# Kernel optimization log

Hardware: AMD Instinct MI355X
Metric: run time of the kernel (lower is better)

Reference implementation:

```python
import jax, jax.numpy as jnp
import numpy as np

B = 32768   # batch of states (original forward is per-state; we vmap)
D = 3       # coord_dim

_W_SHAPES = [("w_h0",(3,32)),("w_y0",(3,32)),("w_yu0",(3,3)),("w_u0",(3,32)),
             ("w_h1",(32,32)),("w_z1",(32,32)),("w_zu1",(32,32)),("w_y1",(3,32)),
             ("w_yu1",(32,3)),("w_u1",(32,32)),("w_h2",(32,32)),("w_z2",(32,32)),
             ("w_zu2",(32,32)),("w_y2",(3,32)),("w_yu2",(32,3)),("w_u2",(32,32)),
             ("w_z_out",(32,1)),("w_zu_out",(32,32)),("w_y_out",(3,1)),
             ("w_yu_out",(32,3)),("w_u_out",(32,1))]
_B_SHAPES = [("b_y0",(3,)),("b_h0",(32,)),("b_0",(32,)),("b_h1",(32,)),("b_y1",(3,)),
             ("b_z1",(32,)),("b_1",(32,)),("b_h2",(32,)),("b_z2",(32,)),("b_y2",(3,)),
             ("b_2",(32,)),("b_z_out",(32,)),("b_y_out",(3,)),("b_out",(1,))]

def _make_params(key):
    n = len(_W_SHAPES) + len(_B_SHAPES) + 4
    ks = jax.random.split(key, n)
    p, i = {}, 0
    for name, sh in _W_SHAPES:   # torch .uniform_(-0.1, 0.1)
        p[name] = jax.random.uniform(ks[i], sh, jnp.float32, -0.1, 0.1); i += 1
    for name, sh in _B_SHAPES:   # torch.rand -> U[0,1)
        p[name] = jax.random.uniform(ks[i], sh, jnp.float32, 0.0, 1.0); i += 1
    # fc layers: normal init per _init_weights (stds / sqrt(16)=4), zero bias
    stds = [2.2/4.0, 0.58/4.0, 0.58*2.0/4.0, 4.0]
    shapes = [(32, 3), (32, 32), (32, 32), (1, 32)]
    for j in range(4):
        p[f"fc{j+1}_w"] = stds[j] * jax.random.normal(ks[i], shapes[j], jnp.float32); i += 1
        p[f"fc{j+1}_b"] = jnp.zeros((shapes[j][0],), jnp.float32)
    return p

def setup_inputs():
    key = jax.random.key(0)
    kx, kp = jax.random.split(key)
    inp = {"x": jax.random.normal(kx, (B, 2 * D), jnp.float32)}
    inp.update(_make_params(kp))
    return inp

def _forward(x, p):
    sp, relu = jax.nn.softplus, jax.nn.relu

    def lagr(state):
        q, y = state[:D], state[D:]
        u1 = sp(q @ p["w_h0"] + p["b_h0"])
        z1 = sp((y * (q @ p["w_yu0"] + p["b_y0"])) @ p["w_y0"] + q @ p["w_u0"] + p["b_0"])
        u2 = sp(u1 @ p["w_h1"] + p["b_h1"])
        z2 = sp((z1 * (u1 @ p["w_zu1"] + p["b_z1"])) @ relu(p["w_z1"])
                + (y * (u1 @ p["w_yu1"] + p["b_y1"])) @ p["w_y1"]
                + u1 @ p["w_u1"] + p["b_1"])
        u3 = sp(u2 @ p["w_h2"] + p["b_h2"])
        z3 = sp((z2 * (u2 @ p["w_zu2"] + p["b_z2"])) @ relu(p["w_z2"])
                + (y * (u2 @ p["w_yu2"] + p["b_y2"])) @ p["w_y2"]
                + u2 @ p["w_u2"] + p["b_2"])
        zout = sp((z3 * (u3 @ p["w_zu_out"] + p["b_z_out"])) @ relu(p["w_z_out"])
                  + (y * (u3 @ p["w_yu_out"] + p["b_y_out"])) @ p["w_y_out"]
                  + u3 @ p["w_u_out"] + p["b_out"])
        V = sp(q @ p["fc1_w"].T + p["fc1_b"])
        V = sp(V @ p["fc2_w"].T + p["fc2_b"])
        V = sp(V @ p["fc3_w"].T + p["fc3_b"])
        V = V @ p["fc4_w"].T + p["fc4_b"]
        return (zout - V)[0]  # scalar Lagrangian

    def step(state):
        dq = state[D:]
        H = jax.hessian(lagr)(state)        # (6,6)
        g = jax.grad(lagr)(state)[:D]       # dL/dq, matches jacobian row b[0,:3]
        M = H[D:, D:]                       # d2L/ddq ddq
        C = H[D:, :D]                       # d2L/ddq dq
        ddq = (g - dq @ C.T) @ jnp.linalg.inv(M).T
        dx = jnp.concatenate([dq, ddq])
        return state + 0.001 * dx           # Euler step, as in torch forward

    return jax.vmap(step)(x)

def reference(x, w_h0, w_y0, w_yu0, w_u0, w_h1, w_z1, w_zu1, w_y1, w_yu1, w_u1,
              w_h2, w_z2, w_zu2, w_y2, w_yu2, w_u2, w_z_out, w_zu_out, w_y_out,
              w_yu_out, w_u_out, b_y0, b_h0, b_0, b_h1, b_y1, b_z1, b_1, b_h2,
              b_z2, b_y2, b_2, b_z_out, b_y_out, b_out, fc1_w, fc1_b, fc2_w,
              fc2_b, fc3_w, fc3_b, fc4_w, fc4_b):
    p = dict(locals())
    xv = p.pop("x")
    return _forward(xv, p)
```

## Files before the change

### kernel.cpp

```cpp
#include <hip/hip_runtime.h>

#define NTH 64
#define B_TOTAL 32768
#define PSTR 20

typedef float v2f __attribute__((ext_vector_type(2)));
typedef float v4f __attribute__((ext_vector_type(4)));
typedef double v4d __attribute__((ext_vector_type(4)));

struct Ptrs { const float* p[44]; };

enum : int {
  I_X = 0,
  I_WH0 = 1, I_WY0 = 2, I_WYU0 = 3, I_WU0 = 4,
  I_WH1 = 5, I_WZ1 = 6, I_WZU1 = 7, I_WY1 = 8, I_WYU1 = 9, I_WU1 = 10,
  I_WH2 = 11, I_WZ2 = 12, I_WZU2 = 13, I_WY2 = 14, I_WYU2 = 15, I_WU2 = 16,
  I_WZO = 17, I_WZUO = 18, I_WYO = 19, I_WYUO = 20, I_WUO = 21,
  I_BY0 = 22, I_BH0 = 23, I_B0 = 24, I_BH1 = 25, I_BY1 = 26, I_BZ1 = 27, I_B1 = 28,
  I_BH2 = 29, I_BZ2 = 30, I_BY2 = 31, I_B2 = 32, I_BZO = 33, I_BYO = 34, I_BOUT = 35,
  I_FC1 = 36, I_FC1B = 37, I_FC2 = 38, I_FC2B = 39, I_FC3 = 40, I_FC3B = 41,
  I_FC4 = 42, I_FC4B = 43
};

struct V16 { float c[16]; };

__device__ __forceinline__ float spf(float x) {
  return fmaxf(x, 0.0f) + __logf(1.0f + __expf(-fabsf(x)));
}
__device__ __forceinline__ float sigf(float x) {
  return __fdividef(1.0f, 1.0f + __expf(-x));
}

__device__ __forceinline__ V16 spchain16(const V16& A, float y0, float y1, float y2) {
  V16 Z;
  float s = sigf(A.c[0]);
  float d = s * (1.0f - s);
  Z.c[0] = spf(A.c[0]);
#pragma unroll
  for (int a = 0; a < 3; ++a) Z.c[1 + a] = s * A.c[1 + a];
#pragma unroll
  for (int b = 0; b < 3; ++b) Z.c[4 + b] = s * A.c[4 + b];
  Z.c[7]  = s * A.c[7]  + d * A.c[1] * A.c[1];
  Z.c[8]  = s * A.c[8]  + d * A.c[1] * A.c[2];
  Z.c[9]  = s * A.c[9]  + d * A.c[1] * A.c[3];
  Z.c[10] = s * A.c[10] + d * A.c[2] * A.c[2];
  Z.c[11] = s * A.c[11] + d * A.c[2] * A.c[3];
  Z.c[12] = s * A.c[12] + d * A.c[3] * A.c[3];
  float ydq = y0 * A.c[4] + y1 * A.c[5] + y2 * A.c[6];
#pragma unroll
  for (int a = 0; a < 3; ++a) Z.c[13 + a] = s * A.c[13 + a] + d * A.c[1 + a] * ydq;
  return Z;
}

__device__ __forceinline__ void stageProd(float* row, const V16& Z, float S0, float S1,
                                          float S2, float S3, float y0, float y1, float y2) {
  float z0 = Z.c[0];
  float ysd = y0 * S1 + y1 * S2 + y2 * S3;
  v4f w0 = {z0 * S0, S0 * Z.c[1], S0 * Z.c[2], S0 * Z.c[3]};
  v4f w1 = {z0 * S1 + S0 * Z.c[4], z0 * S2 + S0 * Z.c[5], z0 * S3 + S0 * Z.c[6], S0 * Z.c[7]};
  v4f w2 = {S0 * Z.c[8], S0 * Z.c[9], S0 * Z.c[10], S0 * Z.c[11]};
  v4f w3 = {S0 * Z.c[12], S0 * Z.c[13] + Z.c[1] * ysd, S0 * Z.c[14] + Z.c[2] * ysd,
            S0 * Z.c[15] + Z.c[3] * ysd};
  *(v4f*)(row + 0) = w0;  *(v4f*)(row + 4) = w1;
  *(v4f*)(row + 8) = w2;  *(v4f*)(row + 12) = w3;
}

__device__ __forceinline__ V16 prodZS16(const V16& Z, float S0, float S1, float S2, float S3,
                                        float y0, float y1, float y2) {
  V16 P;
  const float Sq[3] = {S1, S2, S3};
  float ysd = y0 * S1 + y1 * S2 + y2 * S3;
  P.c[0] = Z.c[0] * S0;
#pragma unroll
  for (int a = 0; a < 3; ++a) P.c[1 + a] = S0 * Z.c[1 + a];
#pragma unroll
  for (int b = 0; b < 3; ++b) P.c[4 + b] = Z.c[0] * Sq[b] + S0 * Z.c[4 + b];
#pragma unroll
  for (int t = 0; t < 6; ++t) P.c[7 + t] = S0 * Z.c[7 + t];
#pragma unroll
  for (int a = 0; a < 3; ++a) P.c[13 + a] = S0 * Z.c[13 + a] + Z.c[1 + a] * ysd;
  return P;
}

__device__ __forceinline__ void stageU_all(const float* __restrict__ Wh,
                                           const float* __restrict__ Wzu,
                                           const float* __restrict__ Wu,
                                           const float* __restrict__ Wyu, int j,
                                           const float* us,
                                           v2f& h0, v2f& h1, v2f& s0, v2f& s1,
                                           v2f& w0, v2f& w1,
                                           v2f& ta0, v2f& ta1, v2f& tb0, v2f& tb1,
                                           v2f& tc0, v2f& tc1) {
#pragma unroll 2
  for (int i = 0; i < 32; ++i) {
    v4f u = *(const v4f*)(us + i * 4);
    float wh = Wh[i * 32 + j], wz = Wzu[i * 32 + j], wu = Wu[i * 32 + j];
    h0 += u.xy * wh; h1 += u.zw * wh;
    s0 += u.xy * wz; s1 += u.zw * wz;
    w0 += u.xy * wu; w1 += u.zw * wu;
    float wy0 = Wyu[i * 3 + 0], wy1 = Wyu[i * 3 + 1], wy2 = Wyu[i * 3 + 2];
    ta0 += u.xy * wy0; ta1 += u.zw * wy0;
    tb0 += u.xy * wy1; tb1 += u.zw * wy1;
    tc0 += u.xy * wy2; tc1 += u.zw * wy2;
  }
}

__device__ __forceinline__ void buildA16(const float* __restrict__ Wy, int j, float y0, float y1,
                                         float y2, const float wv[4], const float ta[4],
                                         const float tb[4], const float tc[4], V16& A) {
  float wy0 = Wy[j], wy1 = Wy[32 + j], wy2 = Wy[64 + j];
  A.c[0] = wv[0] + y0 * ta[0] * wy0 + y1 * tb[0] * wy1 + y2 * tc[0] * wy2;
  A.c[1] = ta[0] * wy0; A.c[2] = tb[0] * wy1; A.c[3] = tc[0] * wy2;
#pragma unroll
  for (int b = 0; b < 3; ++b)
    A.c[4 + b] = wv[1 + b] + y0 * ta[1 + b] * wy0 + y1 * tb[1 + b] * wy1 + y2 * tc[1 + b] * wy2;
#pragma unroll
  for (int t6 = 0; t6 < 6; ++t6) A.c[7 + t6] = 0.0f;
  float yta = y0 * ta[1] + y1 * ta[2] + y2 * ta[3];
  float ytb = y0 * tb[1] + y1 * tb[2] + y2 * tb[3];
  float ytc = y0 * tc[1] + y1 * tc[2] + y2 * tc[3];
  A.c[13] = yta * wy0; A.c[14] = ytb * wy1; A.c[15] = ytc * wy2;
}

__global__ __launch_bounds__(NTH, 4) void lnn_step_kernel(Ptrs P, float* __restrict__ out) {
  __shared__ float pstage[2][32][PSTR];
  __shared__ float ustage[2][32][4];

  const int tid = threadIdx.x;
  const int j = tid & 31;
  const int half = tid >> 5;
  const int sample = blockIdx.x * 2 + half;

  float* prow = &pstage[half][0][0];
  float* urow = &ustage[half][0][0];
  float* pst0 = &pstage[0][0][0];
  float* pst1 = &pstage[1][0][0];
  const int l64 = tid & 63;
  const int n16 = l64 & 15;
  const int kq = l64 >> 4;

  const float* X = P.p[I_X] + sample * 6;
  const float q0 = X[0], q1 = X[1], q2 = X[2];
  const float y0 = X[3], y1 = X[4], y2 = X[5];

  float Vg0, Vg1, Vg2;
  {
    const float* fc1 = P.p[I_FC1];
    float f0 = fc1[j * 3], f1 = fc1[j * 3 + 1], f2 = fc1[j * 3 + 2];
    float hp = P.p[I_FC1B][j] + q0 * f0 + q1 * f1 + q2 * f2;
    float ss = sigf(hp);
    *(v4f*)(urow + j * 4) = (v4f){spf(hp), ss * f0, ss * f1, ss * f2};
    const float* fc2 = P.p[I_FC2] + j * 32;
    v2f a0 = {P.p[I_FC2B][j], 0.0f}, a1 = {0.0f, 0.0f};
#pragma unroll 2
    for (int r = 0; r < 8; ++r) {
      v4f w4 = *(const v4f*)(fc2 + r * 4);
      v4f u0 = *(const v4f*)(urow + (r * 4 + 0) * 4);
      v4f u1 = *(const v4f*)(urow + (r * 4 + 1) * 4);
      v4f u2 = *(const v4f*)(urow + (r * 4 + 2) * 4);
      v4f u3 = *(const v4f*)(urow + (r * 4 + 3) * 4);
      a0 += u0.xy * w4.x; a1 += u0.zw * w4.x;
      a0 += u1.xy * w4.y; a1 += u1.zw * w4.y;
      a0 += u2.xy * w4.z; a1 += u2.zw * w4.z;
      a0 += u3.xy * w4.w; a1 += u3.zw * w4.w;
    }
    float ss2 = sigf(a0.x);
    *(v4f*)(urow + j * 4) = (v4f){spf(a0.x), ss2 * a0.y, ss2 * a1.x, ss2 * a1.y};
    const float* fc3 = P.p[I_FC3] + j * 32;
    v2f b0 = {P.p[I_FC3B][j], 0.0f}, b1 = {0.0f, 0.0f};
#pragma unroll 2
    for (int r = 0; r < 8; ++r) {
      v4f w4 = *(const v4f*)(fc3 + r * 4);
      v4f u0 = *(const v4f*)(urow + (r * 4 + 0) * 4);
      v4f u1 = *(const v4f*)(urow + (r * 4 + 1) * 4);
      v4f u2 = *(const v4f*)(urow + (r * 4 + 2) * 4);
      v4f u3 = *(const v4f*)(urow + (r * 4 + 3) * 4);
      b0 += u0.xy * w4.x; b1 += u0.zw * w4.x;
      b0 += u1.xy * w4.y; b1 += u1.zw * w4.y;
      b0 += u2.xy * w4.z; b1 += u2.zw * w4.z;
      b0 += u3.xy * w4.w; b1 += u3.zw * w4.w;
    }
    float ss3 = sigf(b0.x);
    float f4 = P.p[I_FC4][j];
    Vg0 = ss3 * b0.y * f4; Vg1 = ss3 * b1.x * f4; Vg2 = ss3 * b1.y * f4;
  }

  const float* yu0 = P.p[I_WYU0];
  float t0v[3];
#pragma unroll
  for (int k = 0; k < 3; ++k)
    t0v[k] = q0 * yu0[k] + q1 * yu0[3 + k] + q2 * yu0[6 + k] + P.p[I_BY0][k];

  float u1c[4];
  {
    const float* wh0 = P.p[I_WH0];
    float w0 = wh0[j], w1 = wh0[32 + j], w2 = wh0[64 + j];
    float h = P.p[I_BH0][j] + q0 * w0 + q1 * w1 + q2 * w2;
    float ss = sigf(h);
    u1c[0] = spf(h); u1c[1] = ss * w0; u1c[2] = ss * w1; u1c[3] = ss * w2;
  }

  V16 z;
  {
    const float* Wy = P.p[I_WY0];
    const float* Wu = P.p[I_WU0];
    float wy0 = Wy[j], wy1 = Wy[32 + j], wy2 = Wy[64 + j];
    float wu0 = Wu[j], wu1 = Wu[32 + j], wu2 = Wu[64 + j];
    V16 A;
    A.c[0] = P.p[I_B0][j] + (y0 * t0v[0]) * wy0 + (y1 * t0v[1]) * wy1 + (y2 * t0v[2]) * wy2 +
             q0 * wu0 + q1 * wu1 + q2 * wu2;
    A.c[1] = t0v[0] * wy0; A.c[2] = t0v[1] * wy1; A.c[3] = t0v[2] * wy2;
#pragma unroll
    for (int b = 0; b < 3; ++b) {
      float acc = (b == 0 ? wu0 : (b == 1 ? wu1 : wu2));
      acc += y0 * yu0[b * 3 + 0] * wy0 + y1 * yu0[b * 3 + 1] * wy1 + y2 * yu0[b * 3 + 2] * wy2;
      A.c[4 + b] = acc;
    }
#pragma unroll
    for (int t = 0; t < 6; ++t) A.c[7 + t] = 0.0f;
    float yty0 = y0 * yu0[0] + y1 * yu0[3] + y2 * yu0[6];
    float yty1 = y0 * yu0[1] + y1 * yu0[4] + y2 * yu0[7];
    float yty2 = y0 * yu0[2] + y1 * yu0[5] + y2 * yu0[8];
    A.c[13] = yty0 * wy0; A.c[14] = yty1 * wy1; A.c[15] = yty2 * wy2;
    z = spchain16(A, y0, y1, y2);
  }

  float unext[4];
#pragma unroll 1
  for (int lvl = 0; lvl < 2; ++lvl) {
    const float* Wh  = P.p[lvl == 0 ? I_WH1 : I_WH2];
    const float* Wzu = P.p[lvl == 0 ? I_WZU1 : I_WZU2];
    const float* Wu  = P.p[lvl == 0 ? I_WU1 : I_WU2];
    const float* Wyu = P.p[lvl == 0 ? I_WYU1 : I_WYU2];
    const float* Wy  = P.p[lvl == 0 ? I_WY1 : I_WY2];
    const float* Wz  = P.p[lvl == 0 ? I_WZ1 : I_WZ2];
    const float* Bh  = P.p[lvl == 0 ? I_BH1 : I_BH2];
    const float* Bz  = P.p[lvl == 0 ? I_BZ1 : I_BZ2];
    const float* Bl  = P.p[lvl == 0 ? I_B1 : I_B2];
    const float* By  = P.p[lvl == 0 ? I_BY1 : I_BY2];

    const float* uc = (lvl == 0) ? u1c : unext;
    *(v4f*)(urow + j * 4) = (v4f){uc[0], uc[1], uc[2], uc[3]};

    v2f h0 = {Bh[j], 0.0f}, h1 = {0.0f, 0.0f};
    v2f s0 = {Bz[j], 0.0f}, s1 = {0.0f, 0.0f};
    v2f w0 = {Bl[j], 0.0f}, w1 = {0.0f, 0.0f};
    v2f ta0 = {By[0], 0.0f}, ta1 = {0.0f, 0.0f};
    v2f tb0 = {By[1], 0.0f}, tb1 = {0.0f, 0.0f};
    v2f tc0 = {By[2], 0.0f}, tc1 = {0.0f, 0.0f};
    stageU_all(Wh, Wzu, Wu, Wyu, j, urow, h0, h1, s0, s1, w0, w1,
               ta0, ta1, tb0, tb1, tc0, tc1);
    {
      float ss = sigf(h0.x);
      unext[0] = spf(h0.x); unext[1] = ss * h0.y; unext[2] = ss * h1.x; unext[3] = ss * h1.y;
    }
    stageProd(prow + j * PSTR, z, s0.x, s0.y, s1.x, s1.y, y0, y1, y2);

    v4d a00 = {0.0, 0.0, 0.0, 0.0};
    v4d a01 = {0.0, 0.0, 0.0, 0.0};
    v4d a10 = {0.0, 0.0, 0.0, 0.0};
    v4d a11 = {0.0, 0.0, 0.0, 0.0};
#pragma unroll
    for (int c = 0; c < 8; ++c) {
      const int i = c * 4 + kq;
      double b0 = (double)pst0[i * PSTR + n16];
      double b1 = (double)pst1[i * PSTR + n16];
      double wlo = (double)fmaxf(Wz[i * 32 + n16], 0.0f);
      double whi = (double)fmaxf(Wz[i * 32 + 16 + n16], 0.0f);
      a00 = __builtin_amdgcn_mfma_f64_16x16x4f64(wlo, b0, a00, 0, 0, 0);
      a01 = __builtin_amdgcn_mfma_f64_16x16x4f64(whi, b0, a01, 0, 0, 0);
      a10 = __builtin_amdgcn_mfma_f64_16x16x4f64(wlo, b1, a10, 0, 0, 0);
      a11 = __builtin_amdgcn_mfma_f64_16x16x4f64(whi, b1, a11, 0, 0, 0);
    }
#pragma unroll
    for (int r = 0; r < 4; ++r) {
      pst0[(kq + 4 * r) * PSTR + n16]        = (float)a00[r];
      pst0[(16 + kq + 4 * r) * PSTR + n16]   = (float)a01[r];
      pst1[(kq + 4 * r) * PSTR + n16]        = (float)a10[r];
      pst1[(16 + kq + 4 * r) * PSTR + n16]   = (float)a11[r];
    }

    float wvv[4] = {w0.x, w0.y, w1.x, w1.y};
    float tav[4] = {ta0.x, ta0.y, ta1.x, ta1.y};
    float tbv[4] = {tb0.x, tb0.y, tb1.x, tb1.y};
    float tcv[4] = {tc0.x, tc0.y, tc1.x, tc1.y};
    V16 A2;
    buildA16(Wy, j, y0, y1, y2, wvv, tav, tbv, tcv, A2);

    {
      const float* rown = prow + j * PSTR;
      v4f r0 = *(const v4f*)(rown + 0);
      v4f r1 = *(const v4f*)(rown + 4);
      v4f r2 = *(const v4f*)(rown + 8);
      v4f r3 = *(const v4f*)(rown + 12);
      A2.c[0] += r0.x;  A2.c[1] += r0.y;  A2.c[2] += r0.z;  A2.c[3] += r0.w;
      A2.c[4] += r1.x;  A2.c[5] += r1.y;  A2.c[6] += r1.z;  A2.c[7] += r1.w;
      A2.c[8] += r2.x;  A2.c[9] += r2.y;  A2.c[10] += r2.z; A2.c[11] += r2.w;
      A2.c[12] += r3.x; A2.c[13] += r3.y; A2.c[14] += r3.z; A2.c[15] += r3.w;
    }
    z = spchain16(A2, y0, y1, y2);
  }

  *(v4f*)(urow + j * 4) = (v4f){unext[0], unext[1], unext[2], unext[3]};
  v2f s30 = {P.p[I_BZO][j], 0.0f}, s31 = {0.0f, 0.0f};
  v2f wo0 = {0.0f, 0.0f}, wo1 = {0.0f, 0.0f};
  v2f t3a0 = {P.p[I_BYO][0], 0.0f}, t3a1 = {0.0f, 0.0f};
  v2f t3b0 = {P.p[I_BYO][1], 0.0f}, t3b1 = {0.0f, 0.0f};
  v2f t3c0 = {P.p[I_BYO][2], 0.0f}, t3c1 = {0.0f, 0.0f};
  {
    const float* Wzuo = P.p[I_WZUO];
    const float* Wuo = P.p[I_WUO];
    const float* Wyuo = P.p[I_WYUO];
#pragma unroll 2
    for (int i = 0; i < 32; ++i) {
      v4f u = *(const v4f*)(urow + i * 4);
      float wz = Wzuo[i * 32 + j];
      s30 += u.xy * wz; s31 += u.zw * wz;
      float wu = Wuo[i];
      wo0 += u.xy * wu; wo1 += u.zw * wu;
      float wy0 = Wyuo[i * 3], wy1 = Wyuo[i * 3 + 1], wy2 = Wyuo[i * 3 + 2];
      t3a0 += u.xy * wy0; t3a1 += u.zw * wy0;
      t3b0 += u.xy * wy1; t3b1 += u.zw * wy1;
      t3c0 += u.xy * wy2; t3c1 += u.zw * wy2;
    }
  }
  const float woc[4] = {wo0.x, wo0.y, wo1.x, wo1.y};
  const float t3av[4] = {t3a0.x, t3a0.y, t3a1.x, t3a1.y};
  const float t3bv[4] = {t3b0.x, t3b0.y, t3b1.x, t3b1.y};
  const float t3cv[4] = {t3c0.x, t3c0.y, t3c1.x, t3c1.y};

  float red[19];
  {
    V16 p3 = prodZS16(z, s30.x, s30.y, s31.x, s31.y, y0, y1, y2);
    float wz = fmaxf(P.p[I_WZO][j], 0.0f);
#pragma unroll
    for (int k = 0; k < 16; ++k) red[k] = p3.c[k] * wz;
    red[16] = Vg0; red[17] = Vg1; red[18] = Vg2;
  }
#pragma unroll
  for (int m = 16; m >= 1; m >>= 1) {
#pragma unroll
    for (int k = 0; k < 19; ++k) red[k] += __shfl_xor(red[k], m, 32);
  }

  if (j == 0) {
    const float* Wyo = P.p[I_WYO];
    const float wyo0 = Wyo[0], wyo1 = Wyo[1], wyo2 = Wyo[2];
    float Av = red[0] + woc[0] + P.p[I_BOUT][0] + y0 * t3av[0] * wyo0 +
               y1 * t3bv[0] * wyo1 + y2 * t3cv[0] * wyo2;
    float Agy[3];
    Agy[0] = red[1] + t3av[0] * wyo0;
    Agy[1] = red[2] + t3bv[0] * wyo1;
    Agy[2] = red[3] + t3cv[0] * wyo2;
    float Agq[3];
#pragma unroll
    for (int b = 0; b < 3; ++b)
      Agq[b] = red[4 + b] + woc[1 + b] + y0 * t3av[1 + b] * wyo0 +
               y1 * t3bv[1 + b] * wyo1 + y2 * t3cv[1 + b] * wyo2;
    float ycq[3];
    ycq[0] = red[13] + (y0 * t3av[1] + y1 * t3av[2] + y2 * t3av[3]) * wyo0;
    ycq[1] = red[14] + (y0 * t3bv[1] + y1 * t3bv[2] + y2 * t3bv[3]) * wyo1;
    ycq[2] = red[15] + (y0 * t3cv[1] + y1 * t3cv[2] + y2 * t3cv[3]) * wyo2;
    float s = sigf(Av), d = s * (1.0f - s);

    double Mm[3][3];
    const int pa[6] = {0, 0, 0, 1, 1, 2}, pb[6] = {0, 1, 2, 1, 2, 2};
#pragma unroll
    for (int t = 0; t < 6; ++t) {
      double m = (double)s * (double)red[7 + t] +
                 (double)d * (double)Agy[pa[t]] * (double)Agy[pb[t]];
      Mm[pa[t]][pb[t]] = m; Mm[pb[t]][pa[t]] = m;
    }
    double yAgq = (double)y0 * (double)Agq[0] + (double)y1 * (double)Agq[1] +
                  (double)y2 * (double)Agq[2];
    double rr[3];
#pragma unroll
    for (int a = 0; a < 3; ++a) {
      double g = (double)s * (double)Agq[a] - (double)red[16 + a];
      double Cy = (double)s * (double)ycq[a] + (double)d * (double)Agy[a] * yAgq;
      rr[a] = g - Cy;
    }
    double a = Mm[0][0], b_ = Mm[0][1], c_ = Mm[0][2], dd = Mm[1][1], e = Mm[1][2], f = Mm[2][2];
    double A00 = dd * f - e * e, A01 = c_ * e - b_ * f, A02 = b_ * e - c_ * dd;
    double A11 = a * f - c_ * c_, A12 = b_ * c_ - a * e, A22 = a * dd - b_ * b_;
    double det = a * A00 + b_ * A01 + c_ * A02;
    double idet = 1.0 / det;
    double d0 = (A00 * rr[0] + A01 * rr[1] + A02 * rr[2]) * idet;
    double d1 = (A01 * rr[0] + A11 * rr[1] + A12 * rr[2]) * idet;
    double d2 = (A02 * rr[0] + A12 * rr[1] + A22 * rr[2]) * idet;

    float* O = out + (size_t)sample * 6;
    O[0] = q0 + 0.001f * y0;
    O[1] = q1 + 0.001f * y1;
    O[2] = q2 + 0.001f * y2;
    O[3] = y0 + 0.001f * (float)d0;
    O[4] = y1 + 0.001f * (float)d1;
    O[5] = y2 + 0.001f * (float)d2;
  }
}

extern "C" void kernel_launch(void* const* d_in, const int* in_sizes, int n_in,
                              void* d_out, int out_size, void* d_ws, size_t ws_size,
                              hipStream_t stream) {
  (void)in_sizes; (void)n_in; (void)d_ws; (void)ws_size; (void)out_size;
  Ptrs P;
  for (int i = 0; i < 44; ++i) P.p[i] = (const float*)d_in[i];
  float* out = (float*)d_out;
  dim3 grid(B_TOTAL / 2), block(NTH);
  hipLaunchKernelGGL(lnn_step_kernel, grid, block, 0, stream, P, out);
}
```

Measured before the change: 130.6 us.

## Process two samples per half-wave to amortize weight loads and MFMA work

Each 32-lane half now handles two samples instead of one, so a 64-thread block covers four samples and the grid is halved. The Wz matrix loads are reused across two MFMA pairs, and per-sample phases are factored into inline helpers. The launch-bounds occupancy hint of 4 is dropped. Live registers per thread roughly double with two V16 states, which may cut occupancy or cause spills, and the serialized per-sample work gives less parallelism per block.

```diff
diff --git a/kernel.cpp b/kernel.cpp
--- a/kernel.cpp
+++ b/kernel.cpp
@@ -122,110 +122,256 @@
   A.c[13] = yta * wy0; A.c[14] = ytb * wy1; A.c[15] = ytc * wy2;
 }
 
-__global__ __launch_bounds__(NTH, 4) void lnn_step_kernel(Ptrs P, float* __restrict__ out) {
-  __shared__ float pstage[2][32][PSTR];
-  __shared__ float ustage[2][32][4];
+__device__ __forceinline__ void vchainVALU(const Ptrs& P, int j, float q0, float q1, float q2,
+                                           float* urow, float& Vg0, float& Vg1, float& Vg2) {
+  const float* fc1 = P.p[I_FC1];
+  float f0 = fc1[j * 3], f1 = fc1[j * 3 + 1], f2 = fc1[j * 3 + 2];
+  float hp = P.p[I_FC1B][j] + q0 * f0 + q1 * f1 + q2 * f2;
+  float ss = sigf(hp);
+  *(v4f*)(urow + j * 4) = (v4f){spf(hp), ss * f0, ss * f1, ss * f2};
+  const float* fc2 = P.p[I_FC2] + j * 32;
+  v2f a0 = {P.p[I_FC2B][j], 0.0f}, a1 = {0.0f, 0.0f};
+#pragma unroll 2
+  for (int r = 0; r < 8; ++r) {
+    v4f w4 = *(const v4f*)(fc2 + r * 4);
+    v4f u0 = *(const v4f*)(urow + (r * 4 + 0) * 4);
+    v4f u1 = *(const v4f*)(urow + (r * 4 + 1) * 4);
+    v4f u2 = *(const v4f*)(urow + (r * 4 + 2) * 4);
+    v4f u3 = *(const v4f*)(urow + (r * 4 + 3) * 4);
+    a0 += u0.xy * w4.x; a1 += u0.zw * w4.x;
+    a0 += u1.xy * w4.y; a1 += u1.zw * w4.y;
+    a0 += u2.xy * w4.z; a1 += u2.zw * w4.z;
+    a0 += u3.xy * w4.w; a1 += u3.zw * w4.w;
+  }
+  float ss2 = sigf(a0.x);
+  *(v4f*)(urow + j * 4) = (v4f){spf(a0.x), ss2 * a0.y, ss2 * a1.x, ss2 * a1.y};
+  const float* fc3 = P.p[I_FC3] + j * 32;
+  v2f b0 = {P.p[I_FC3B][j], 0.0f}, b1 = {0.0f, 0.0f};
+#pragma unroll 2
+  for (int r = 0; r < 8; ++r) {
+    v4f w4 = *(const v4f*)(fc3 + r * 4);
+    v4f u0 = *(const v4f*)(urow + (r * 4 + 0) * 4);
+    v4f u1 = *(const v4f*)(urow + (r * 4 + 1) * 4);
+    v4f u2 = *(const v4f*)(urow + (r * 4 + 2) * 4);
+    v4f u3 = *(const v4f*)(urow + (r * 4 + 3) * 4);
+    b0 += u0.xy * w4.x; b1 += u0.zw * w4.x;
+    b0 += u1.xy * w4.y; b1 += u1.zw * w4.y;
+    b0 += u2.xy * w4.z; b1 += u2.zw * w4.z;
+    b0 += u3.xy * w4.w; b1 += u3.zw * w4.w;
+  }
+  float ss3 = sigf(b0.x);
+  float f4 = P.p[I_FC4][j];
+  Vg0 = ss3 * b0.y * f4; Vg1 = ss3 * b1.x * f4; Vg2 = ss3 * b1.y * f4;
+}
+
+__device__ __forceinline__ V16 zinit(const Ptrs& P, int j, float q0, float q1, float q2,
+                                     float y0, float y1, float y2) {
+  const float* yu0 = P.p[I_WYU0];
+  float t0v[3];
+#pragma unroll
+  for (int k = 0; k < 3; ++k)
+    t0v[k] = q0 * yu0[k] + q1 * yu0[3 + k] + q2 * yu0[6 + k] + P.p[I_BY0][k];
+  const float* Wy = P.p[I_WY0];
+  const float* Wu = P.p[I_WU0];
+  float wy0 = Wy[j], wy1 = Wy[32 + j], wy2 = Wy[64 + j];
+  float wu0 = Wu[j], wu1 = Wu[32 + j], wu2 = Wu[64 + j];
+  V16 A;
+  A.c[0] = P.p[I_B0][j] + (y0 * t0v[0]) * wy0 + (y1 * t0v[1]) * wy1 + (y2 * t0v[2]) * wy2 +
+           q0 * wu0 + q1 * wu1 + q2 * wu2;
+  A.c[1] = t0v[0] * wy0; A.c[2] = t0v[1] * wy1; A.c[3] = t0v[2] * wy2;
+#pragma unroll
+  for (int b = 0; b < 3; ++b) {
+    float acc = (b == 0 ? wu0 : (b == 1 ? wu1 : wu2));
+    acc += y0 * yu0[b * 3 + 0] * wy0 + y1 * yu0[b * 3 + 1] * wy1 + y2 * yu0[b * 3 + 2] * wy2;
+    A.c[4 + b] = acc;
+  }
+#pragma unroll
+  for (int t = 0; t < 6; ++t) A.c[7 + t] = 0.0f;
+  float yty0 = y0 * yu0[0] + y1 * yu0[3] + y2 * yu0[6];
+  float yty1 = y0 * yu0[1] + y1 * yu0[4] + y2 * yu0[7];
+  float yty2 = y0 * yu0[2] + y1 * yu0[5] + y2 * yu0[8];
+  A.c[13] = yty0 * wy0; A.c[14] = yty1 * wy1; A.c[15] = yty2 * wy2;
+  return spchain16(A, y0, y1, y2);
+}
+
+__device__ __forceinline__ void u1init(const Ptrs& P, int j, float q0, float q1, float q2,
+                                       float u1c[4]) {
+  const float* wh0 = P.p[I_WH0];
+  float w0 = wh0[j], w1 = wh0[32 + j], w2 = wh0[64 + j];
+  float h = P.p[I_BH0][j] + q0 * w0 + q1 * w1 + q2 * w2;
+  float ss = sigf(h);
+  u1c[0] = spf(h); u1c[1] = ss * w0; u1c[2] = ss * w1; u1c[3] = ss * w2;
+}
+
+__device__ __forceinline__ void mv16pair(const float* __restrict__ Wz, int n16, int kq,
+                                         float* pstX, float* pstY) {
+  v4d a00 = {0.0, 0.0, 0.0, 0.0};
+  v4d a01 = {0.0, 0.0, 0.0, 0.0};
+  v4d a10 = {0.0, 0.0, 0.0, 0.0};
+  v4d a11 = {0.0, 0.0, 0.0, 0.0};
+#pragma unroll
+  for (int c = 0; c < 8; ++c) {
+    const int i = c * 4 + kq;
+    double b0 = (double)pstX[i * PSTR + n16];
+    double b1 = (double)pstY[i * PSTR + n16];
+    double wlo = (double)fmaxf(Wz[i * 32 + n16], 0.0f);
+    double whi = (double)fmaxf(Wz[i * 32 + 16 + n16], 0.0f);
+    a00 = __builtin_amdgcn_mfma_f64_16x16x4f64(wlo, b0, a00, 0, 0, 0);
+    a01 = __builtin_amdgcn_mfma_f64_16x16x4f64(whi, b0, a01, 0, 0, 0);
+    a10 = __builtin_amdgcn_mfma_f64_16x16x4f64(wlo, b1, a10, 0, 0, 0);
+    a11 = __builtin_amdgcn_mfma_f64_16x16x4f64(whi, b1, a11, 0, 0, 0);
+  }
+#pragma unroll
+  for (int r = 0; r < 4; ++r) {
+    pstX[(kq + 4 * r) * PSTR + n16]      = (float)a00[r];
+    pstX[(16 + kq + 4 * r) * PSTR + n16] = (float)a01[r];
+    pstY[(kq + 4 * r) * PSTR + n16]      = (float)a10[r];
+    pstY[(16 + kq + 4 * r) * PSTR + n16] = (float)a11[r];
+  }
+}
+
+__device__ __forceinline__ void level3VALU(const Ptrs& P, int j, const float* urow,
+                                           float s3c[4], float t3av[4], float t3bv[4],
+                                           float t3cv[4], float woc[4]) {
+  v2f s30 = {P.p[I_BZO][j], 0.0f}, s31 = {0.0f, 0.0f};
+  v2f wo0 = {0.0f, 0.0f}, wo1 = {0.0f, 0.0f};
+  v2f t3a0 = {P.p[I_BYO][0], 0.0f}, t3a1 = {0.0f, 0.0f};
+  v2f t3b0 = {P.p[I_BYO][1], 0.0f}, t3b1 = {0.0f, 0.0f};
+  v2f t3c0 = {P.p[I_BYO][2], 0.0f}, t3c1 = {0.0f, 0.0f};
+  const float* Wzuo = P.p[I_WZUO];
+  const float* Wuo = P.p[I_WUO];
+  const float* Wyuo = P.p[I_WYUO];
+#pragma unroll 2
+  for (int i = 0; i < 32; ++i) {
+    v4f u = *(const v4f*)(urow + i * 4);
+    float wz = Wzuo[i * 32 + j];
+    s30 += u.xy * wz; s31 += u.zw * wz;
+    float wu = Wuo[i];
+    wo0 += u.xy * wu; wo1 += u.zw * wu;
+    float wy0 = Wyuo[i * 3], wy1 = Wyuo[i * 3 + 1], wy2 = Wyuo[i * 3 + 2];
+    t3a0 += u.xy * wy0; t3a1 += u.zw * wy0;
+    t3b0 += u.xy * wy1; t3b1 += u.zw * wy1;
+    t3c0 += u.xy * wy2; t3c1 += u.zw * wy2;
+  }
+  s3c[0] = s30.x; s3c[1] = s30.y; s3c[2] = s31.x; s3c[3] = s31.y;
+  woc[0] = wo0.x; woc[1] = wo0.y; woc[2] = wo1.x; woc[3] = wo1.y;
+  t3av[0] = t3a0.x; t3av[1] = t3a0.y; t3av[2] = t3a1.x; t3av[3] = t3a1.y;
+  t3bv[0] = t3b0.x; t3bv[1] = t3b0.y; t3bv[2] = t3b1.x; t3bv[3] = t3b1.y;
+  t3cv[0] = t3c0.x; t3cv[1] = t3c0.y; t3cv[2] = t3c1.x; t3cv[3] = t3c1.y;
+}
+
+__device__ __forceinline__ void finishSample(const Ptrs& P, int j, const V16& z,
+                                             const float s3c[4], const float t3av[4],
+                                             const float t3bv[4], const float t3cv[4],
+                                             const float woc[4], float Vg0, float Vg1, float Vg2,
+                                             float q0, float q1, float q2, float y0, float y1,
+                                             float y2, float* __restrict__ out, int sample) {
+  float red[19];
+  {
+    V16 p3 = prodZS16(z, s3c[0], s3c[1], s3c[2], s3c[3], y0, y1, y2);
+    float wz = fmaxf(P.p[I_WZO][j], 0.0f);
+#pragma unroll
+    for (int k = 0; k < 16; ++k) red[k] = p3.c[k] * wz;
+    red[16] = Vg0; red[17] = Vg1; red[18] = Vg2;
+  }
+#pragma unroll
+  for (int m = 16; m >= 1; m >>= 1) {
+#pragma unroll
+    for (int k = 0; k < 19; ++k) red[k] += __shfl_xor(red[k], m, 32);
+  }
+  if (j == 0) {
+    const float* Wyo = P.p[I_WYO];
+    const float wyo0 = Wyo[0], wyo1 = Wyo[1], wyo2 = Wyo[2];
+    float Av = red[0] + woc[0] + P.p[I_BOUT][0] + y0 * t3av[0] * wyo0 +
+               y1 * t3bv[0] * wyo1 + y2 * t3cv[0] * wyo2;
+    float Agy[3];
+    Agy[0] = red[1] + t3av[0] * wyo0;
+    Agy[1] = red[2] + t3bv[0] * wyo1;
+    Agy[2] = red[3] + t3cv[0] * wyo2;
+    float Agq[3];
+#pragma unroll
+    for (int b = 0; b < 3; ++b)
+      Agq[b] = red[4 + b] + woc[1 + b] + y0 * t3av[1 + b] * wyo0 +
+               y1 * t3bv[1 + b] * wyo1 + y2 * t3cv[1 + b] * wyo2;
+    float ycq[3];
+    ycq[0] = red[13] + (y0 * t3av[1] + y1 * t3av[2] + y2 * t3av[3]) * wyo0;
+    ycq[1] = red[14] + (y0 * t3bv[1] + y1 * t3bv[2] + y2 * t3bv[3]) * wyo1;
+    ycq[2] = red[15] + (y0 * t3cv[1] + y1 * t3cv[2] + y2 * t3cv[3]) * wyo2;
+    float s = sigf(Av), d = s * (1.0f - s);
+    double Mm[3][3];
+    const int pa[6] = {0, 0, 0, 1, 1, 2}, pb[6] = {0, 1, 2, 1, 2, 2};
+#pragma unroll
+    for (int t = 0; t < 6; ++t) {
+      double m = (double)s * (double)red[7 + t] +
+                 (double)d * (double)Agy[pa[t]] * (double)Agy[pb[t]];
+      Mm[pa[t]][pb[t]] = m; Mm[pb[t]][pa[t]] = m;
+    }
+    double yAgq = (double)y0 * (double)Agq[0] + (double)y1 * (double)Agq[1] +
+                  (double)y2 * (double)Agq[2];
+    double rr[3];
+#pragma unroll
+    for (int a = 0; a < 3; ++a) {
+      double g = (double)s * (double)Agq[a] - (double)red[16 + a];
+      double Cy = (double)s * (double)ycq[a] + (double)d * (double)Agy[a] * yAgq;
+      rr[a] = g - Cy;
+    }
+    double a = Mm[0][0], b_ = Mm[0][1], c_ = Mm[0][2], dd = Mm[1][1], e = Mm[1][2], f = Mm[2][2];
+    double A00 = dd * f - e * e, A01 = c_ * e - b_ * f, A02 = b_ * e - c_ * dd;
+    double A11 = a * f - c_ * c_, A12 = b_ * c_ - a * e, A22 = a * dd - b_ * b_;
+    double det = a * A00 + b_ * A01 + c_ * A02;
+    double idet = 1.0 / det;
+    double d0 = (A00 * rr[0] + A01 * rr[1] + A02 * rr[2]) * idet;
+    double d1 = (A01 * rr[0] + A11 * rr[1] + A12 * rr[2]) * idet;
+    double d2 = (A02 * rr[0] + A12 * rr[1] + A22 * rr[2]) * idet;
+    float* O = out + (size_t)sample * 6;
+    O[0] = q0 + 0.001f * y0;
+    O[1] = q1 + 0.001f * y1;
+    O[2] = q2 + 0.001f * y2;
+    O[3] = y0 + 0.001f * (float)d0;
+    O[4] = y1 + 0.001f * (float)d1;
+    O[5] = y2 + 0.001f * (float)d2;
+  }
+}
+
+__global__ __launch_bounds__(NTH) void lnn_step_kernel(Ptrs P, float* __restrict__ out) {
+  __shared__ float pstage[4][32][PSTR];
+  __shared__ float ustage[4][32][4];
 
   const int tid = threadIdx.x;
   const int j = tid & 31;
   const int half = tid >> 5;
-  const int sample = blockIdx.x * 2 + half;
-
-  float* prow = &pstage[half][0][0];
-  float* urow = &ustage[half][0][0];
+  const int sA = blockIdx.x * 4 + half * 2;
+  const int sB = sA + 1;
+
+  float* prowA = &pstage[half * 2 + 0][0][0];
+  float* prowB = &pstage[half * 2 + 1][0][0];
+  float* urowA = &ustage[half * 2 + 0][0][0];
+  float* urowB = &ustage[half * 2 + 1][0][0];
   float* pst0 = &pstage[0][0][0];
   float* pst1 = &pstage[1][0][0];
+  float* pst2 = &pstage[2][0][0];
+  float* pst3 = &pstage[3][0][0];
   const int l64 = tid & 63;
   const int n16 = l64 & 15;
   const int kq = l64 >> 4;
 
-  const float* X = P.p[I_X] + sample * 6;
-  const float q0 = X[0], q1 = X[1], q2 = X[2];
-  const float y0 = X[3], y1 = X[4], y2 = X[5];
-
-  float Vg0, Vg1, Vg2;
-  {
-    const float* fc1 = P.p[I_FC1];
-    float f0 = fc1[j * 3], f1 = fc1[j * 3 + 1], f2 = fc1[j * 3 + 2];
-    float hp = P.p[I_FC1B][j] + q0 * f0 + q1 * f1 + q2 * f2;
-    float ss = sigf(hp);
-    *(v4f*)(urow + j * 4) = (v4f){spf(hp), ss * f0, ss * f1, ss * f2};
-    const float* fc2 = P.p[I_FC2] + j * 32;
-    v2f a0 = {P.p[I_FC2B][j], 0.0f}, a1 = {0.0f, 0.0f};
-#pragma unroll 2
-    for (int r = 0; r < 8; ++r) {
-      v4f w4 = *(const v4f*)(fc2 + r * 4);
-      v4f u0 = *(const v4f*)(urow + (r * 4 + 0) * 4);
-      v4f u1 = *(const v4f*)(urow + (r * 4 + 1) * 4);
-      v4f u2 = *(const v4f*)(urow + (r * 4 + 2) * 4);
-      v4f u3 = *(const v4f*)(urow + (r * 4 + 3) * 4);
-      a0 += u0.xy * w4.x; a1 += u0.zw * w4.x;
-      a0 += u1.xy * w4.y; a1 += u1.zw * w4.y;
-      a0 += u2.xy * w4.z; a1 += u2.zw * w4.z;
-      a0 += u3.xy * w4.w; a1 += u3.zw * w4.w;
-    }
-    float ss2 = sigf(a0.x);
-    *(v4f*)(urow + j * 4) = (v4f){spf(a0.x), ss2 * a0.y, ss2 * a1.x, ss2 * a1.y};
-    const float* fc3 = P.p[I_FC3] + j * 32;
-    v2f b0 = {P.p[I_FC3B][j], 0.0f}, b1 = {0.0f, 0.0f};
-#pragma unroll 2
-    for (int r = 0; r < 8; ++r) {
-      v4f w4 = *(const v4f*)(fc3 + r * 4);
-      v4f u0 = *(const v4f*)(urow + (r * 4 + 0) * 4);
-      v4f u1 = *(const v4f*)(urow + (r * 4 + 1) * 4);
-      v4f u2 = *(const v4f*)(urow + (r * 4 + 2) * 4);
-      v4f u3 = *(const v4f*)(urow + (r * 4 + 3) * 4);
-      b0 += u0.xy * w4.x; b1 += u0.zw * w4.x;
-      b0 += u1.xy * w4.y; b1 += u1.zw * w4.y;
-      b0 += u2.xy * w4.z; b1 += u2.zw * w4.z;
-      b0 += u3.xy * w4.w; b1 += u3.zw * w4.w;
-    }
-    float ss3 = sigf(b0.x);
-    float f4 = P.p[I_FC4][j];
-    Vg0 = ss3 * b0.y * f4; Vg1 = ss3 * b1.x * f4; Vg2 = ss3 * b1.y * f4;
-  }
-
-  const float* yu0 = P.p[I_WYU0];
-  float t0v[3];
-#pragma unroll
-  for (int k = 0; k < 3; ++k)
-    t0v[k] = q0 * yu0[k] + q1 * yu0[3 + k] + q2 * yu0[6 + k] + P.p[I_BY0][k];
-
-  float u1c[4];
-  {
-    const float* wh0 = P.p[I_WH0];
-    float w0 = wh0[j], w1 = wh0[32 + j], w2 = wh0[64 + j];
-    float h = P.p[I_BH0][j] + q0 * w0 + q1 * w1 + q2 * w2;
-    float ss = sigf(h);
-    u1c[0] = spf(h); u1c[1] = ss * w0; u1c[2] = ss * w1; u1c[3] = ss * w2;
-  }
-
-  V16 z;
-  {
-    const float* Wy = P.p[I_WY0];
-    const float* Wu = P.p[I_WU0];
-    float wy0 = Wy[j], wy1 = Wy[32 + j], wy2 = Wy[64 + j];
-    float wu0 = Wu[j], wu1 = Wu[32 + j], wu2 = Wu[64 + j];
-    V16 A;
-    A.c[0] = P.p[I_B0][j] + (y0 * t0v[0]) * wy0 + (y1 * t0v[1]) * wy1 + (y2 * t0v[2]) * wy2 +
-             q0 * wu0 + q1 * wu1 + q2 * wu2;
-    A.c[1] = t0v[0] * wy0; A.c[2] = t0v[1] * wy1; A.c[3] = t0v[2] * wy2;
-#pragma unroll
-    for (int b = 0; b < 3; ++b) {
-      float acc = (b == 0 ? wu0 : (b == 1 ? wu1 : wu2));
-      acc += y0 * yu0[b * 3 + 0] * wy0 + y1 * yu0[b * 3 + 1] * wy1 + y2 * yu0[b * 3 + 2] * wy2;
-      A.c[4 + b] = acc;
-    }
-#pragma unroll
-    for (int t = 0; t < 6; ++t) A.c[7 + t] = 0.0f;
-    float yty0 = y0 * yu0[0] + y1 * yu0[3] + y2 * yu0[6];
-    float yty1 = y0 * yu0[1] + y1 * yu0[4] + y2 * yu0[7];
-    float yty2 = y0 * yu0[2] + y1 * yu0[5] + y2 * yu0[8];
-    A.c[13] = yty0 * wy0; A.c[14] = yty1 * wy1; A.c[15] = yty2 * wy2;
-    z = spchain16(A, y0, y1, y2);
-  }
-
-  float unext[4];
+  const float* XA = P.p[I_X] + (size_t)sA * 6;
+  const float* XB = P.p[I_X] + (size_t)sB * 6;
+  const float qA0 = XA[0], qA1 = XA[1], qA2 = XA[2];
+  const float yA0 = XA[3], yA1 = XA[4], yA2 = XA[5];
+  const float qB0 = XB[0], qB1 = XB[1], qB2 = XB[2];
+  const float yB0 = XB[3], yB1 = XB[4], yB2 = XB[5];
+
+  float VgA0, VgA1, VgA2, VgB0, VgB1, VgB2;
+  vchainVALU(P, j, qA0, qA1, qA2, urowA, VgA0, VgA1, VgA2);
+  vchainVALU(P, j, qB0, qB1, qB2, urowB, VgB0, VgB1, VgB2);
+
+  float uA[4], uB[4];
+  u1init(P, j, qA0, qA1, qA2, uA);
+  u1init(P, j, qB0, qB1, qB2, uB);
+  V16 zA = zinit(P, j, qA0, qA1, qA2, yA0, yA1, yA2);
+  V16 zB = zinit(P, j, qB0, qB1, qB2, yB0, yB1, yB2);
+
 #pragma unroll 1
   for (int lvl = 0; lvl < 2; ++lvl) {
     const float* Wh  = P.p[lvl == 0 ? I_WH1 : I_WH2];
@@ -239,163 +385,88 @@
     const float* Bl  = P.p[lvl == 0 ? I_B1 : I_B2];
     const float* By  = P.p[lvl == 0 ? I_BY1 : I_BY2];
 
-    const float* uc = (lvl == 0) ? u1c : unext;
-    *(v4f*)(urow + j * 4) = (v4f){uc[0], uc[1], uc[2], uc[3]};
-
-    v2f h0 = {Bh[j], 0.0f}, h1 = {0.0f, 0.0f};
-    v2f s0 = {Bz[j], 0.0f}, s1 = {0.0f, 0.0f};
-    v2f w0 = {Bl[j], 0.0f}, w1 = {0.0f, 0.0f};
-    v2f ta0 = {By[0], 0.0f}, ta1 = {0.0f, 0.0f};
-    v2f tb0 = {By[1], 0.0f}, tb1 = {0.0f, 0.0f};
-    v2f tc0 = {By[2], 0.0f}, tc1 = {0.0f, 0.0f};
-    stageU_all(Wh, Wzu, Wu, Wyu, j, urow, h0, h1, s0, s1, w0, w1,
-               ta0, ta1, tb0, tb1, tc0, tc1);
+    V16 A2A, A2B;
     {
+      *(v4f*)(urowA + j * 4) = (v4f){uA[0], uA[1], uA[2], uA[3]};
+      v2f h0 = {Bh[j], 0.0f}, h1 = {0.0f, 0.0f};
+      v2f s0 = {Bz[j], 0.0f}, s1 = {0.0f, 0.0f};
+      v2f w0 = {Bl[j], 0.0f}, w1 = {0.0f, 0.0f};
+      v2f ta0 = {By[0], 0.0f}, ta1 = {0.0f, 0.0f};
+      v2f tb0 = {By[1], 0.0f}, tb1 = {0.0f, 0.0f};
+      v2f tc0 = {By[2], 0.0f}, tc1 = {0.0f, 0.0f};
+      stageU_all(Wh, Wzu, Wu, Wyu, j, urowA, h0, h1, s0, s1, w0, w1,
+                 ta0, ta1, tb0, tb1, tc0, tc1);
       float ss = sigf(h0.x);
-      unext[0] = spf(h0.x); unext[1] = ss * h0.y; unext[2] = ss * h1.x; unext[3] = ss * h1.y;
-    }
-    stageProd(prow + j * PSTR, z, s0.x, s0.y, s1.x, s1.y, y0, y1, y2);
-
-    v4d a00 = {0.0, 0.0, 0.0, 0.0};
-    v4d a01 = {0.0, 0.0, 0.0, 0.0};
-    v4d a10 = {0.0, 0.0, 0.0, 0.0};
-    v4d a11 = {0.0, 0.0, 0.0, 0.0};
-#pragma unroll
-    for (int c = 0; c < 8; ++c) {
-      const int i = c * 4 + kq;
-      double b0 = (double)pst0[i * PSTR + n16];
-      double b1 = (double)pst1[i * PSTR + n16];
-      double wlo = (double)fmaxf(Wz[i * 32 + n16], 0.0f);
-      double whi = (double)fmaxf(Wz[i * 32 + 16 + n16], 0.0f);
-      a00 = __builtin_amdgcn_mfma_f64_16x16x4f64(wlo, b0, a00, 0, 0, 0);
-      a01 = __builtin_amdgcn_mfma_f64_16x16x4f64(whi, b0, a01, 0, 0, 0);
-      a10 = __builtin_amdgcn_mfma_f64_16x16x4f64(wlo, b1, a10, 0, 0, 0);
-      a11 = __builtin_amdgcn_mfma_f64_16x16x4f64(whi, b1, a11, 0, 0, 0);
-    }
-#pragma unroll
-    for (int r = 0; r < 4; ++r) {
-      pst0[(kq + 4 * r) * PSTR + n16]        = (float)a00[r];
-      pst0[(16 + kq + 4 * r) * PSTR + n16]   = (float)a01[r];
-      pst1[(kq + 4 * r) * PSTR + n16]        = (float)a10[r];
-      pst1[(16 + kq + 4 * r) * PSTR + n16]   = (float)a11[r];
-    }
-
-    float wvv[4] = {w0.x, w0.y, w1.x, w1.y};
-    float tav[4] = {ta0.x, ta0.y, ta1.x, ta1.y};
-    float tbv[4] = {tb0.x, tb0.y, tb1.x, tb1.y};
-    float tcv[4] = {tc0.x, tc0.y, tc1.x, tc1.y};
-    V16 A2;
-    buildA16(Wy, j, y0, y1, y2, wvv, tav, tbv, tcv, A2);
-
+      uA[0] = spf(h0.x); uA[1] = ss * h0.y; uA[2] = ss * h1.x; uA[3] = ss * h1.y;
+      stageProd(prowA + j * PSTR, zA, s0.x, s0.y, s1.x, s1.y, yA0, yA1, yA2);
+      float wvv[4] = {w0.x, w0.y, w1.x, w1.y};
+      float tav[4] = {ta0.x, ta0.y, ta1.x, ta1.y};
+      float tbv[4] = {tb0.x, tb0.y, tb1.x, tb1.y};
+      float tcv[4] = {tc0.x, tc0.y, tc1.x, tc1.y};
+      buildA16(Wy, j, yA0, yA1, yA2, wvv, tav, tbv, tcv, A2A);
+    }
     {
-      const float* rown = prow + j * PSTR;
+      *(v4f*)(urowB + j * 4) = (v4f){uB[0], uB[1], uB[2], uB[3]};
+      v2f h0 = {Bh[j], 0.0f}, h1 = {0.0f, 0.0f};
+      v2f s0 = {Bz[j], 0.0f}, s1 = {0.0f, 0.0f};
+      v2f w0 = {Bl[j], 0.0f}, w1 = {0.0f, 0.0f};
+      v2f ta0 = {By[0], 0.0f}, ta1 = {0.0f, 0.0f};
+      v2f tb0 = {By[1], 0.0f}, tb1 = {0.0f, 0.0f};
+      v2f tc0 = {By[2], 0.0f}, tc1 = {0.0f, 0.0f};
+      stageU_all(Wh, Wzu, Wu, Wyu, j, urowB, h0, h1, s0, s1, w0, w1,
+                 ta0, ta1, tb0, tb1, tc0, tc1);
+      float ss = sigf(h0.x);
+      uB[0] = spf(h0.x); uB[1] = ss * h0.y; uB[2] = ss * h1.x; uB[3] = ss * h1.y;
+      stageProd(prowB + j * PSTR, zB, s0.x, s0.y, s1.x, s1.y, yB0, yB1, yB2);
+      float wvv[4] = {w0.x, w0.y, w1.x, w1.y};
+      float tav[4] = {ta0.x, ta0.y, ta1.x, ta1.y};
+      float tbv[4] = {tb0.x, tb0.y, tb1.x, tb1.y};
+      float tcv[4] = {tc0.x, tc0.y, tc1.x, tc1.y};
+      buildA16(Wy, j, yB0, yB1, yB2, wvv, tav, tbv, tcv, A2B);
+    }
+
+    mv16pair(Wz, n16, kq, pst0, pst1);
+    mv16pair(Wz, n16, kq, pst2, pst3);
+
+    {
+      const float* rown = prowA + j * PSTR;
       v4f r0 = *(const v4f*)(rown + 0);
       v4f r1 = *(const v4f*)(rown + 4);
       v4f r2 = *(const v4f*)(rown + 8);
       v4f r3 = *(const v4f*)(rown + 12);
-      A2.c[0] += r0.x;  A2.c[1] += r0.y;  A2.c[2] += r0.z;  A2.c[3] += r0.w;
-      A2.c[4] += r1.x;  A2.c[5] += r1.y;  A2.c[6] += r1.z;  A2.c[7] += r1.w;
-      A2.c[8] += r2.x;  A2.c[9] += r2.y;  A2.c[10] += r2.z; A2.c[11] += r2.w;
-      A2.c[12] += r3.x; A2.c[13] += r3.y; A2.c[14] += r3.z; A2.c[15] += r3.w;
-    }
-    z = spchain16(A2, y0, y1, y2);
-  }
-
-  *(v4f*)(urow + j * 4) = (v4f){unext[0], unext[1], unext[2], unext[3]};
-  v2f s30 = {P.p[I_BZO][j], 0.0f}, s31 = {0.0f, 0.0f};
-  v2f wo0 = {0.0f, 0.0f}, wo1 = {0.0f, 0.0f};
-  v2f t3a0 = {P.p[I_BYO][0], 0.0f}, t3a1 = {0.0f, 0.0f};
-  v2f t3b0 = {P.p[I_BYO][1], 0.0f}, t3b1 = {0.0f, 0.0f};
-  v2f t3c0 = {P.p[I_BYO][2], 0.0f}, t3c1 = {0.0f, 0.0f};
+      A2A.c[0] += r0.x;  A2A.c[1] += r0.y;  A2A.c[2] += r0.z;  A2A.c[3] += r0.w;
+      A2A.c[4] += r1.x;  A2A.c[5] += r1.y;  A2A.c[6] += r1.z;  A2A.c[7] += r1.w;
+      A2A.c[8] += r2.x;  A2A.c[9] += r2.y;  A2A.c[10] += r2.z; A2A.c[11] += r2.w;
+      A2A.c[12] += r3.x; A2A.c[13] += r3.y; A2A.c[14] += r3.z; A2A.c[15] += r3.w;
+    }
+    zA = spchain16(A2A, yA0, yA1, yA2);
+    {
+      const float* rown = prowB + j * PSTR;
+      v4f r0 = *(const v4f*)(rown + 0);
+      v4f r1 = *(const v4f*)(rown + 4);
+      v4f r2 = *(const v4f*)(rown + 8);
+      v4f r3 = *(const v4f*)(rown + 12);
+      A2B.c[0] += r0.x;  A2B.c[1] += r0.y;  A2B.c[2] += r0.z;  A2B.c[3] += r0.w;
+      A2B.c[4] += r1.x;  A2B.c[5] += r1.y;  A2B.c[6] += r1.z;  A2B.c[7] += r1.w;
+      A2B.c[8] += r2.x;  A2B.c[9] += r2.y;  A2B.c[10] += r2.z; A2B.c[11] += r2.w;
+      A2B.c[12] += r3.x; A2B.c[13] += r3.y; A2B.c[14] += r3.z; A2B.c[15] += r3.w;
+    }
+    zB = spchain16(A2B, yB0, yB1, yB2);
+  }
+
+  *(v4f*)(urowA + j * 4) = (v4f){uA[0], uA[1], uA[2], uA[3]};
+  *(v4f*)(urowB + j * 4) = (v4f){uB[0], uB[1], uB[2], uB[3]};
   {
-    const float* Wzuo = P.p[I_WZUO];
-    const float* Wuo = P.p[I_WUO];
-    const float* Wyuo = P.p[I_WYUO];
-#pragma unroll 2
-    for (int i = 0; i < 32; ++i) {
-      v4f u = *(const v4f*)(urow + i * 4);
-      float wz = Wzuo[i * 32 + j];
-      s30 += u.xy * wz; s31 += u.zw * wz;
-      float wu = Wuo[i];
-      wo0 += u.xy * wu; wo1 += u.zw * wu;
-      float wy0 = Wyuo[i * 3], wy1 = Wyuo[i * 3 + 1], wy2 = Wyuo[i * 3 + 2];
-      t3a0 += u.xy * wy0; t3a1 += u.zw * wy0;
-      t3b0 += u.xy * wy1; t3b1 += u.zw * wy1;
-      t3c0 += u.xy * wy2; t3c1 += u.zw * wy2;
-    }
-  }
-  const float woc[4] = {wo0.x, wo0.y, wo1.x, wo1.y};
-  const float t3av[4] = {t3a0.x, t3a0.y, t3a1.x, t3a1.y};
-  const float t3bv[4] = {t3b0.x, t3b0.y, t3b1.x, t3b1.y};
-  const float t3cv[4] = {t3c0.x, t3c0.y, t3c1.x, t3c1.y};
-
-  float red[19];
+    float s3c[4], t3av[4], t3bv[4], t3cv[4], woc[4];
+    level3VALU(P, j, urowA, s3c, t3av, t3bv, t3cv, woc);
+    finishSample(P, j, zA, s3c, t3av, t3bv, t3cv, woc, VgA0, VgA1, VgA2,
+                 qA0, qA1, qA2, yA0, yA1, yA2, out, sA);
+  }
   {
-    V16 p3 = prodZS16(z, s30.x, s30.y, s31.x, s31.y, y0, y1, y2);
-    float wz = fmaxf(P.p[I_WZO][j], 0.0f);
-#pragma unroll
-    for (int k = 0; k < 16; ++k) red[k] = p3.c[k] * wz;
-    red[16] = Vg0; red[17] = Vg1; red[18] = Vg2;
-  }
-#pragma unroll
-  for (int m = 16; m >= 1; m >>= 1) {
-#pragma unroll
-    for (int k = 0; k < 19; ++k) red[k] += __shfl_xor(red[k], m, 32);
-  }
-
-  if (j == 0) {
-    const float* Wyo = P.p[I_WYO];
-    const float wyo0 = Wyo[0], wyo1 = Wyo[1], wyo2 = Wyo[2];
-    float Av = red[0] + woc[0] + P.p[I_BOUT][0] + y0 * t3av[0] * wyo0 +
-               y1 * t3bv[0] * wyo1 + y2 * t3cv[0] * wyo2;
-    float Agy[3];
-    Agy[0] = red[1] + t3av[0] * wyo0;
-    Agy[1] = red[2] + t3bv[0] * wyo1;
-    Agy[2] = red[3] + t3cv[0] * wyo2;
-    float Agq[3];
-#pragma unroll
-    for (int b = 0; b < 3; ++b)
-      Agq[b] = red[4 + b] + woc[1 + b] + y0 * t3av[1 + b] * wyo0 +
-               y1 * t3bv[1 + b] * wyo1 + y2 * t3cv[1 + b] * wyo2;
-    float ycq[3];
-    ycq[0] = red[13] + (y0 * t3av[1] + y1 * t3av[2] + y2 * t3av[3]) * wyo0;
-    ycq[1] = red[14] + (y0 * t3bv[1] + y1 * t3bv[2] + y2 * t3bv[3]) * wyo1;
-    ycq[2] = red[15] + (y0 * t3cv[1] + y1 * t3cv[2] + y2 * t3cv[3]) * wyo2;
-    float s = sigf(Av), d = s * (1.0f - s);
-
-    double Mm[3][3];
-    const int pa[6] = {0, 0, 0, 1, 1, 2}, pb[6] = {0, 1, 2, 1, 2, 2};
-#pragma unroll
-    for (int t = 0; t < 6; ++t) {
-      double m = (double)s * (double)red[7 + t] +
-                 (double)d * (double)Agy[pa[t]] * (double)Agy[pb[t]];
-      Mm[pa[t]][pb[t]] = m; Mm[pb[t]][pa[t]] = m;
-    }
-    double yAgq = (double)y0 * (double)Agq[0] + (double)y1 * (double)Agq[1] +
-                  (double)y2 * (double)Agq[2];
-    double rr[3];
-#pragma unroll
-    for (int a = 0; a < 3; ++a) {
-      double g = (double)s * (double)Agq[a] - (double)red[16 + a];
-      double Cy = (double)s * (double)ycq[a] + (double)d * (double)Agy[a] * yAgq;
-      rr[a] = g - Cy;
-    }
-    double a = Mm[0][0], b_ = Mm[0][1], c_ = Mm[0][2], dd = Mm[1][1], e = Mm[1][2], f = Mm[2][2];
-    double A00 = dd * f - e * e, A01 = c_ * e - b_ * f, A02 = b_ * e - c_ * dd;
-    double A11 = a * f - c_ * c_, A12 = b_ * c_ - a * e, A22 = a * dd - b_ * b_;
-    double det = a * A00 + b_ * A01 + c_ * A02;
-    double idet = 1.0 / det;
-    double d0 = (A00 * rr[0] + A01 * rr[1] + A02 * rr[2]) * idet;
-    double d1 = (A01 * rr[0] + A11 * rr[1] + A12 * rr[2]) * idet;
-    double d2 = (A02 * rr[0] + A12 * rr[1] + A22 * rr[2]) * idet;
-
-    float* O = out + (size_t)sample * 6;
-    O[0] = q0 + 0.001f * y0;
-    O[1] = q1 + 0.001f * y1;
-    O[2] = q2 + 0.001f * y2;
-    O[3] = y0 + 0.001f * (float)d0;
-    O[4] = y1 + 0.001f * (float)d1;
-    O[5] = y2 + 0.001f * (float)d2;
+    float s3c[4], t3av[4], t3bv[4], t3cv[4], woc[4];
+    level3VALU(P, j, urowB, s3c, t3av, t3bv, t3cv, woc);
+    finishSample(P, j, zB, s3c, t3av, t3bv, t3cv, woc, VgB0, VgB1, VgB2,
+                 qB0, qB1, qB2, yB0, yB1, yB2, out, sB);
   }
 }
 
@@ -406,6 +477,6 @@
   Ptrs P;
   for (int i = 0; i < 44; ++i) P.p[i] = (const float*)d_in[i];
   float* out = (float*)d_out;
-  dim3 grid(B_TOTAL / 2), block(NTH);
+  dim3 grid(B_TOTAL / 4), block(NTH);
   hipLaunchKernelGGL(lnn_step_kernel, grid, block, 0, stream, P, out);
 }
```

Result: slower. 155.1 us (+18.7%).
